# Optimization experiments

Hardware: AMD Instinct MI355X
Metric: run time of the kernel (lower is better)

## Reference

```python
import jax, jax.numpy as jnp
import numpy as np

K = 16
D_MODEL = 128

def _gather(pts, idx):
    # pts: [B,N,C], idx: [B,N,K] -> [B,N,K,C]
    return jax.vmap(lambda p, i: p[i])(pts, idx)

def setup_inputs() -> dict:
    key = jax.random.key(0)
    ks = jax.random.split(key, 20)
    s = 0.05
    def w(k_, shape):
        return jax.random.normal(k_, shape, dtype=jnp.float32) * s
    B, N, C = 4, 4096, 3
    TF, D = 128, D_MODEL
    return {
        "xyz": jax.random.normal(ks[0], (B, N, C), dtype=jnp.float32),
        "W0a": w(ks[1], (C, TF)),  "b0a": jnp.zeros((TF,), jnp.float32),
        "W0b": w(ks[2], (TF, TF)), "b0b": jnp.zeros((TF,), jnp.float32),
        "W1":  w(ks[3], (TF, D)),  "b1":  jnp.zeros((D,), jnp.float32),
        "W2":  w(ks[4], (D, TF)),  "b2":  jnp.zeros((TF,), jnp.float32),
        "Wd1": w(ks[5], (C, D)),   "bd1": jnp.zeros((D,), jnp.float32),
        "Wd2": w(ks[6], (D, D)),   "bd2": jnp.zeros((D,), jnp.float32),
        "Wg1": w(ks[7], (D, D)),   "bg1": jnp.zeros((D,), jnp.float32),
        "Wg2": w(ks[8], (D, D)),   "bg2": jnp.zeros((D,), jnp.float32),
        "Wq":  w(ks[9], (D, D)),
        "Wk":  w(ks[10], (D, D)),
        "Wv":  w(ks[11], (D, D)),
    }

def reference(xyz, W0a, b0a, W0b, b0b, W1, b1, W2, b2,
              Wd1, bd1, Wd2, bd2, Wg1, bg1, Wg2, bg2, Wq, Wk, Wv):
    sq = jnp.sum(xyz * xyz, axis=-1)
    dists = sq[:, :, None] - 2.0 * jnp.einsum('bnc,bmc->bnm', xyz, xyz) + sq[:, None, :]
    _, knn_idx = jax.lax.top_k(-dists, K)          # [B,N,K] nearest neighbors

    knn_xyz = _gather(xyz, knn_idx)                # [B,N,K,3]
    features = jax.nn.relu(xyz @ W0a + b0a) @ W0b + b0b   # fc0  [B,N,TF]
    pre = features
    x = features @ W1 + b1                          # fc1  [B,N,D]
    q = x @ Wq                                      # [B,N,D]
    kf = _gather(x @ Wk, knn_idx)                   # [B,N,K,D]
    vf = _gather(x @ Wv, knn_idx)                   # [B,N,K,D]

    delta = xyz[:, :, None, :] - knn_xyz            # [B,N,K,3]
    pos_enc = jax.nn.relu(delta @ Wd1 + bd1) @ Wd2 + bd2   # fc_delta [B,N,K,D]

    h = q[:, :, None, :] - kf + pos_enc
    attn_logits = jax.nn.relu(h @ Wg1 + bg1) @ Wg2 + bg2   # fc_gamma [B,N,K,D]
    attn = jax.nn.softmax(attn_logits / np.sqrt(D_MODEL).astype(np.float32), axis=-2)

    res = jnp.einsum('bmnf,bmnf->bmf', attn, vf + pos_enc)  # [B,N,D]
    res = res @ W2 + b2 + pre                               # [B,N,TF]
    return res, attn
```

## Files before the change

kernel.cpp:

```cpp
#include <hip/hip_runtime.h>
#include <math.h>

#define BB 4
#define NN 4096
#define KNNK 16
#define DD 128
#define BN (BB*NN)

typedef __attribute__((ext_vector_type(8))) short short8;
typedef __attribute__((ext_vector_type(4))) float floatx4;

__device__ __forceinline__ short f2bf(float x) {
  unsigned u = __float_as_uint(x);
  unsigned r = (u + 0x7fffu + ((u >> 16) & 1u)) >> 16;
  return (short)r;
}

__device__ __forceinline__ float bf2f(short h) {
  return __uint_as_float((unsigned)(unsigned short)h << 16);
}

__device__ __forceinline__ void mv16(const float* __restrict__ Wcol,
                                     const float* __restrict__ A,
                                     float acc[16]) {
#pragma unroll 2
  for (int f4 = 0; f4 < 32; ++f4) {
    float w0 = Wcol[(4 * f4 + 0) * 128];
    float w1 = Wcol[(4 * f4 + 1) * 128];
    float w2 = Wcol[(4 * f4 + 2) * 128];
    float w3 = Wcol[(4 * f4 + 3) * 128];
#pragma unroll
    for (int p = 0; p < 16; ++p) {
      float4 a = *reinterpret_cast<const float4*>(A + p * 128 + 4 * f4);
      acc[p] = fmaf(a.w, w3, fmaf(a.z, w2, fmaf(a.y, w1, fmaf(a.x, w0, acc[p]))));
    }
  }
}

__device__ __forceinline__ void ced(double& a, double& b) {
  double mn = fmin(a, b);
  double mx = fmax(a, b);
  a = mn;
  b = mx;
}

__device__ __forceinline__ void dsort16(double v[16]) {
#define CE(i, j) ced(v[i], v[j]);
  CE(0, 1) CE(2, 3) CE(4, 5) CE(6, 7) CE(8, 9) CE(10, 11) CE(12, 13) CE(14, 15)
  CE(0, 2) CE(1, 3) CE(4, 6) CE(5, 7) CE(8, 10) CE(9, 11) CE(12, 14) CE(13, 15)
  CE(1, 2) CE(5, 6) CE(9, 10) CE(13, 14)
  CE(0, 4) CE(1, 5) CE(2, 6) CE(3, 7) CE(8, 12) CE(9, 13) CE(10, 14) CE(11, 15)
  CE(2, 4) CE(3, 5) CE(10, 12) CE(11, 13)
  CE(1, 2) CE(3, 4) CE(5, 6) CE(9, 10) CE(11, 12) CE(13, 14)
  CE(0, 8) CE(1, 9) CE(2, 10) CE(3, 11) CE(4, 12) CE(5, 13) CE(6, 14) CE(7, 15)
  CE(4, 8) CE(5, 9) CE(6, 10) CE(7, 11)
  CE(2, 4) CE(3, 5) CE(6, 8) CE(7, 9) CE(10, 12) CE(11, 13)
  CE(1, 2) CE(3, 4) CE(5, 6) CE(7, 8) CE(9, 10) CE(11, 12) CE(13, 14)
#undef CE
}

__device__ __forceinline__ void dbitonic16(double m[16]) {
#pragma unroll
  for (int s = 8; s >= 1; s >>= 1) {
#pragma unroll
    for (int i = 0; i < 16; ++i) {
      if ((i & s) == 0) ced(m[i], m[i + s]);
    }
  }
}

__global__ __launch_bounds__(256, 4) void knn_kernel(const float* __restrict__ xyz,
                                                     int* __restrict__ knn) {
  const int wv = threadIdx.x >> 6;
  const int lane = threadIdx.x & 63;
  const int q = blockIdx.x * 4 + wv;
  const int b = q >> 12;
  const int n = q & 4095;
  const float* xb = xyz + (size_t)b * NN * 3;

  const float qx = xb[n * 3 + 0], qy = xb[n * 3 + 1], qz = xb[n * 3 + 2];
  const float qsq = __fadd_rn(__fadd_rn(__fmul_rn(qx, qx), __fmul_rn(qy, qy)),
                              __fmul_rn(qz, qz));

  double top[16];
#pragma unroll
  for (int batch = 0; batch < 4; ++batch) {
    double v[16];
#pragma unroll
    for (int i = 0; i < 16; ++i) {
      const int c = (batch * 16 + i) * 64 + lane;
      float cx = xb[c * 3 + 0], cy = xb[c * 3 + 1], cz = xb[c * 3 + 2];
      float csq = __fadd_rn(__fadd_rn(__fmul_rn(cx, cx), __fmul_rn(cy, cy)),
                            __fmul_rn(cz, cz));
      float dot = __fadd_rn(__fadd_rn(__fmul_rn(qx, cx), __fmul_rn(qy, cy)),
                            __fmul_rn(qz, cz));
      float d = __fadd_rn(__fsub_rn(qsq, __fmul_rn(2.0f, dot)), csq);
      unsigned u = __float_as_uint(d);
      u = (u & 0x80000000u) ? ~u : (u | 0x80000000u);
      unsigned long long key =
          0x3FF0000000000000ULL | (((unsigned long long)u << 12) | (unsigned)c);
      v[i] = __longlong_as_double((long long)key);
    }
    dsort16(v);
    if (batch == 0) {
#pragma unroll
      for (int i = 0; i < 16; ++i) top[i] = v[i];
    } else {
      double m[16];
#pragma unroll
      for (int i = 0; i < 16; ++i)
        m[i] = fmin(top[i], v[15 - i]);
      dbitonic16(m);
#pragma unroll
      for (int i = 0; i < 16; ++i) top[i] = m[i];
    }
  }

#pragma unroll
  for (int mask = 1; mask <= 32; mask <<= 1) {
    double oth[16];
#pragma unroll
    for (int i = 0; i < 16; ++i) {
      double y = __shfl_xor(top[15 - i], mask);
      oth[i] = fmin(y, top[i]);
    }
    dbitonic16(oth);
#pragma unroll
    for (int i = 0; i < 16; ++i) top[i] = oth[i];
  }

  if (lane == 0) {
    int* outp = knn + (size_t)q * KNNK;
#pragma unroll
    for (int k = 0; k < 16; ++k)
      outp[k] = (int)(__double_as_longlong(top[k]) & 0xFFFLL);
  }
}

__global__ void swz_kernel(const float* __restrict__ Wd2,
                           const float* __restrict__ Wg1,
                           const float* __restrict__ Wg2,
                           short* __restrict__ wsw) {
  int t = blockIdx.x * 256 + threadIdx.x;
  if (t >= 3 * 2048) return;
  int stage = t / 2048;
  int rem = t % 2048;
  int nt = rem / 256;
  int ks = (rem % 256) / 64;
  int lane = rem % 64;
  const float* W = (stage == 0) ? Wd2 : (stage == 1) ? Wg1 : Wg2;
  short8 o;
#pragma unroll
  for (int j = 0; j < 8; ++j) {
    int k = ks * 32 + (lane >> 4) * 8 + j;
    int n = nt * 16 + (lane & 15);
    o[j] = f2bf(W[k * 128 + n]);
  }
  *reinterpret_cast<short8*>(wsw + (size_t)t * 8) = o;
}

__global__ void swz2_kernel(const float* __restrict__ W0b,
                            const float* __restrict__ W1,
                            const float* __restrict__ Wq,
                            const float* __restrict__ Wk,
                            const float* __restrict__ Wv,
                            short* __restrict__ wsplit) {
  int t = blockIdx.x * 256 + threadIdx.x;
  if (t >= 5 * 2048) return;
  int mat = t / 2048;
  int rem = t % 2048;
  int lane = rem % 64;
  const float* W = (mat == 0) ? W0b : (mat == 1) ? W1 : (mat == 2) ? Wq
                   : (mat == 3) ? Wk : Wv;
  short8 hi, lo;
#pragma unroll
  for (int j = 0; j < 8; ++j) {
    int ks = (rem % 256) / 64;
    int nt = rem / 256;
    int k = ks * 32 + (lane >> 4) * 8 + j;
    int n = nt * 16 + (lane & 15);
    float w = W[k * 128 + n];
    short h = f2bf(w);
    hi[j] = h;
    lo[j] = f2bf(w - bf2f(h));
  }
  *reinterpret_cast<short8*>(wsplit + ((size_t)(2 * mat) * 2048 + rem) * 8) = hi;
  *reinterpret_cast<short8*>(wsplit + ((size_t)(2 * mat + 1) * 2048 + rem) * 8) = lo;
}

__global__ __launch_bounds__(256, 4) void point_mlp_mfma_kernel(
    const float* __restrict__ xyz, const float* __restrict__ W0a,
    const float* __restrict__ b0a, const float* __restrict__ b0b,
    const float* __restrict__ b1, const short* __restrict__ wsplit,
    float* __restrict__ pre, float* __restrict__ qv, float* __restrict__ kv,
    float* __restrict__ vv) {
  const int wv = threadIdx.x >> 6;
  const int lane = threadIdx.x & 63;
  const int g = lane >> 4;
  const int c = lane & 15;
  const int g0 = blockIdx.x * 16;
  const int nt0 = wv * 2;

  __shared__ __attribute__((aligned(16))) float trans[16 * 132];
  __shared__ float xs[64];
  if (threadIdx.x < 48) {
    int p = threadIdx.x / 3, cc = threadIdx.x % 3;
    xs[p * 4 + cc] = xyz[(size_t)(g0 + p) * 3 + cc];
  }
  __syncthreads();

  short8 ah[4], al[4];
  {
    const float x0 = xs[c * 4 + 0], x1 = xs[c * 4 + 1], x2 = xs[c * 4 + 2];
#pragma unroll
    for (int s = 0; s < 4; ++s) {
#pragma unroll
      for (int j = 0; j < 8; ++j) {
        const int k = s * 32 + g * 8 + j;
        float v = fmaf(x2, W0a[256 + k],
                       fmaf(x1, W0a[128 + k], fmaf(x0, W0a[k], b0a[k])));
        v = fmaxf(v, 0.f);
        const short h = f2bf(v);
        ah[s][j] = h;
        al[s][j] = f2bf(v - bf2f(h));
      }
    }
  }

#define DOGEMM(mat)                                                            \
  {                                                                            \
    const short* Bh = wsplit + (size_t)(2 * (mat)) * 16384;                    \
    const short* Bl = Bh + 16384;                                              \
    _Pragma("unroll") for (int ks = 0; ks < 4; ++ks) {                         \
      const size_t o0 = ((size_t)((nt0 + 0) * 4 + ks) * 64 + lane) * 8;        \
      const size_t o1 = ((size_t)((nt0 + 1) * 4 + ks) * 64 + lane) * 8;        \
      short8 bh0 = *reinterpret_cast<const short8*>(Bh + o0);                  \
      short8 bl0 = *reinterpret_cast<const short8*>(Bl + o0);                  \
      short8 bh1 = *reinterpret_cast<const short8*>(Bh + o1);                  \
      short8 bl1 = *reinterpret_cast<const short8*>(Bl + o1);                  \
      acc0 = __builtin_amdgcn_mfma_f32_16x16x32_bf16(ah[ks], bh0, acc0, 0, 0, 0); \
      acc1 = __builtin_amdgcn_mfma_f32_16x16x32_bf16(ah[ks], bh1, acc1, 0, 0, 0); \
      acc0 = __builtin_amdgcn_mfma_f32_16x16x32_bf16(ah[ks], bl0, acc0, 0, 0, 0); \
      acc1 = __builtin_amdgcn_mfma_f32_16x16x32_bf16(ah[ks], bl1, acc1, 0, 0, 0); \
      acc0 = __builtin_amdgcn_mfma_f32_16x16x32_bf16(al[ks], bh0, acc0, 0, 0, 0); \
      acc1 = __builtin_amdgcn_mfma_f32_16x16x32_bf16(al[ks], bh1, acc1, 0, 0, 0); \
    }                                                                          \
  }

#define SPLITLD()                                                              \
  _Pragma("unroll") for (int s = 0; s < 4; ++s) {                              \
    const float* p_ = &trans[c * 132 + s * 32 + g * 8];                        \
    float4 u0 = *reinterpret_cast<const float4*>(p_);                          \
    float4 u1 = *reinterpret_cast<const float4*>(p_ + 4);                      \
    float tmp[8] = {u0.x, u0.y, u0.z, u0.w, u1.x, u1.y, u1.z, u1.w};           \
    _Pragma("unroll") for (int j = 0; j < 8; ++j) {                            \
      short h_ = f2bf(tmp[j]);                                                 \
      ah[s][j] = h_;                                                           \
      al[s][j] = f2bf(tmp[j] - bf2f(h_));                                      \
    }                                                                          \
  }

  floatx4 acc0, acc1;
  const floatx4 zf = (floatx4){0.f, 0.f, 0.f, 0.f};

  acc0 = zf; acc1 = zf;
  DOGEMM(0);
  {
    const float bb0 = b0b[nt0 * 16 + c];
    const float bb1 = b0b[(nt0 + 1) * 16 + c];
#pragma unroll
    for (int r = 0; r < 4; ++r) {
      const int row = g * 4 + r;
      float v0 = acc0[r] + bb0;
      float v1 = acc1[r] + bb1;
      pre[(size_t)(g0 + row) * 128 + nt0 * 16 + c] = v0;
      pre[(size_t)(g0 + row) * 128 + (nt0 + 1) * 16 + c] = v1;
      trans[row * 132 + nt0 * 16 + c] = v0;
      trans[row * 132 + (nt0 + 1) * 16 + c] = v1;
    }
  }
  __syncthreads();
  SPLITLD();
  __syncthreads();

  acc0 = zf; acc1 = zf;
  DOGEMM(1);
  {
    const float bb0 = b1[nt0 * 16 + c];
    const float bb1 = b1[(nt0 + 1) * 16 + c];
#pragma unroll
    for (int r = 0; r < 4; ++r) {
      const int row = g * 4 + r;
      trans[row * 132 + nt0 * 16 + c] = acc0[r] + bb0;
      trans[row * 132 + (nt0 + 1) * 16 + c] = acc1[r] + bb1;
    }
  }
  __syncthreads();
  SPLITLD();
  __syncthreads();

#define GSTORE(dst)                                                            \
  _Pragma("unroll") for (int r = 0; r < 4; ++r) {                              \
    const int row = g0 + g * 4 + r;                                            \
    dst[(size_t)row * 128 + nt0 * 16 + c] = acc0[r];                           \
    dst[(size_t)row * 128 + (nt0 + 1) * 16 + c] = acc1[r];                     \
  }

  acc0 = zf; acc1 = zf;
  DOGEMM(2);
  GSTORE(qv);

  acc0 = zf; acc1 = zf;
  DOGEMM(3);
  GSTORE(kv);

  acc0 = zf; acc1 = zf;
  DOGEMM(4);
  GSTORE(vv);

#undef DOGEMM
#undef SPLITLD
#undef GSTORE
}

__global__ __launch_bounds__(256, 2) void attn_mfma_kernel(
    const float* __restrict__ xyz, const int* __restrict__ knn,
    const float* __restrict__ qv, const float* __restrict__ kv,
    const float* __restrict__ vv, const short* __restrict__ wsw,
    const float* __restrict__ Wd1, const float* __restrict__ bd1,
    const float* __restrict__ bd2, const float* __restrict__ bg1,
    const float* __restrict__ bg2, float* __restrict__ res_ws,
    float* __restrict__ out_attn) {
  const int wv = threadIdx.x >> 6;
  const int lane = threadIdx.x & 63;
  const int g = lane >> 4;
  const int c = lane & 15;
  const int bn = blockIdx.x * 4 + wv;
  const int b = bn >> 12;

  __shared__ __attribute__((aligned(16))) short conv[4][16 * 136];
  __shared__ int sidx[4][16];
  __shared__ float sdelta[4][64];

  if (lane < 16) sidx[wv][lane] = knn[(size_t)bn * 16 + lane];
  __syncthreads();
  if (lane < 48) {
    int k = lane / 3, cc = lane % 3;
    sdelta[wv][k * 4 + cc] = xyz[(size_t)bn * 3 + cc] -
                             xyz[((size_t)(b << 12) + sidx[wv][k]) * 3 + cc];
  }
  __syncthreads();

  short8 af[4];
  {
    float ddx = sdelta[wv][c * 4 + 0];
    float ddy = sdelta[wv][c * 4 + 1];
    float ddz = sdelta[wv][c * 4 + 2];
#pragma unroll
    for (int s = 0; s < 4; ++s) {
#pragma unroll
      for (int j = 0; j < 8; ++j) {
        int d = s * 32 + g * 8 + j;
        float v = fmaf(ddz, Wd1[256 + d],
                       fmaf(ddy, Wd1[128 + d], fmaf(ddx, Wd1[d], bd1[d])));
        af[s][j] = f2bf(fmaxf(v, 0.f));
      }
    }
  }

  float qc[8], bd2v[8], bg1v[8], bg2v[8];
#pragma unroll
  for (int nt = 0; nt < 8; ++nt) {
    qc[nt] = qv[(size_t)bn * 128 + nt * 16 + c];
    bd2v[nt] = bd2[nt * 16 + c];
    bg1v[nt] = bg1[nt * 16 + c];
    bg2v[nt] = bg2[nt * 16 + c];
  }

  floatx4 acc[8];

#pragma unroll
  for (int nt = 0; nt < 8; ++nt) acc[nt] = (floatx4){0.f, 0.f, 0.f, 0.f};
  {
    const short* Wst = wsw;
#pragma unroll
    for (int ks = 0; ks < 4; ++ks) {
#pragma unroll
      for (int nt = 0; nt < 8; ++nt) {
        short8 bf = *reinterpret_cast<const short8*>(
            Wst + ((size_t)(nt * 4 + ks) * 64 + lane) * 8);
        acc[nt] = __builtin_amdgcn_mfma_f32_16x16x32_bf16(af[ks], bf, acc[nt],
                                                          0, 0, 0);
      }
    }
  }

  float PE[8][4];
  int idxr[4];
#pragma unroll
  for (int r = 0; r < 4; ++r) idxr[r] = sidx[wv][g * 4 + r];
#pragma unroll
  for (int nt = 0; nt < 8; ++nt) {
#pragma unroll
    for (int r = 0; r < 4; ++r) {
      float pe = acc[nt][r] + bd2v[nt];
      PE[nt][r] = pe;
      float kvv = kv[((size_t)(b << 12) + idxr[r]) * 128 + nt * 16 + c];
      conv[wv][(g * 4 + r) * 136 + nt * 16 + c] = f2bf(qc[nt] - kvv + pe);
    }
  }
  __syncthreads();
#pragma unroll
  for (int s = 0; s < 4; ++s)
    af[s] = *reinterpret_cast<const short8*>(&conv[wv][c * 136 + s * 32 + g * 8]);
  __syncthreads();

#pragma unroll
  for (int nt = 0; nt < 8; ++nt) acc[nt] = (floatx4){0.f, 0.f, 0.f, 0.f};
  {
    const short* Wst = wsw + 16384;
#pragma unroll
    for (int ks = 0; ks < 4; ++ks) {
#pragma unroll
      for (int nt = 0; nt < 8; ++nt) {
        short8 bf = *reinterpret_cast<const short8*>(
            Wst + ((size_t)(nt * 4 + ks) * 64 + lane) * 8);
        acc[nt] = __builtin_amdgcn_mfma_f32_16x16x32_bf16(af[ks], bf, acc[nt],
                                                          0, 0, 0);
      }
    }
  }
#pragma unroll
  for (int nt = 0; nt < 8; ++nt) {
#pragma unroll
    for (int r = 0; r < 4; ++r) {
      conv[wv][(g * 4 + r) * 136 + nt * 16 + c] =
          f2bf(fmaxf(acc[nt][r] + bg1v[nt], 0.f));
    }
  }
  __syncthreads();
#pragma unroll
  for (int s = 0; s < 4; ++s)
    af[s] = *reinterpret_cast<const short8*>(&conv[wv][c * 136 + s * 32 + g * 8]);
  __syncthreads();

#pragma unroll
  for (int nt = 0; nt < 8; ++nt) acc[nt] = (floatx4){0.f, 0.f, 0.f, 0.f};
  {
    const short* Wst = wsw + 32768;
#pragma unroll
    for (int ks = 0; ks < 4; ++ks) {
#pragma unroll
      for (int nt = 0; nt < 8; ++nt) {
        short8 bf = *reinterpret_cast<const short8*>(
            Wst + ((size_t)(nt * 4 + ks) * 64 + lane) * 8);
        acc[nt] = __builtin_amdgcn_mfma_f32_16x16x32_bf16(af[ks], bf, acc[nt],
                                                          0, 0, 0);
      }
    }
  }

  const float inv = 0.0883883476483184f;
  float resv[8];
#pragma unroll
  for (int nt = 0; nt < 8; ++nt) {
    float l0 = (acc[nt][0] + bg2v[nt]) * inv;
    float l1 = (acc[nt][1] + bg2v[nt]) * inv;
    float l2 = (acc[nt][2] + bg2v[nt]) * inv;
    float l3 = (acc[nt][3] + bg2v[nt]) * inv;
    float m4 = fmaxf(fmaxf(l0, l1), fmaxf(l2, l3));
    m4 = fmaxf(m4, __shfl_xor(m4, 16));
    m4 = fmaxf(m4, __shfl_xor(m4, 32));
    float e0 = expf(l0 - m4), e1 = expf(l1 - m4);
    float e2 = expf(l2 - m4), e3 = expf(l3 - m4);
    float s4 = e0 + e1 + e2 + e3;
    s4 += __shfl_xor(s4, 16);
    s4 += __shfl_xor(s4, 32);
    float rs = 1.f / s4;
    float a0 = e0 * rs, a1 = e1 * rs, a2 = e2 * rs, a3 = e3 * rs;
    size_t base = ((size_t)bn * 16 + g * 4) * 128 + nt * 16 + c;
    out_attn[base + 0 * 128] = a0;
    out_attn[base + 1 * 128] = a1;
    out_attn[base + 2 * 128] = a2;
    out_attn[base + 3 * 128] = a3;
    float r = 0.f;
    {
      float v0 = vv[((size_t)(b << 12) + idxr[0]) * 128 + nt * 16 + c];
      float v1 = vv[((size_t)(b << 12) + idxr[1]) * 128 + nt * 16 + c];
      float v2 = vv[((size_t)(b << 12) + idxr[2]) * 128 + nt * 16 + c];
      float v3 = vv[((size_t)(b << 12) + idxr[3]) * 128 + nt * 16 + c];
      r = fmaf(a0, v0 + PE[nt][0], r);
      r = fmaf(a1, v1 + PE[nt][1], r);
      r = fmaf(a2, v2 + PE[nt][2], r);
      r = fmaf(a3, v3 + PE[nt][3], r);
    }
    r += __shfl_xor(r, 16);
    r += __shfl_xor(r, 32);
    resv[nt] = r;
  }
  if (g == 0) {
#pragma unroll
    for (int nt = 0; nt < 8; ++nt)
      res_ws[(size_t)bn * 128 + nt * 16 + c] = resv[nt];
  }
}

__global__ __launch_bounds__(128, 2) void epilogue_kernel(
    const float* __restrict__ res_ws, const float* __restrict__ W2,
    const float* __restrict__ b2, const float* __restrict__ pre,
    float* __restrict__ out_res) {
  const int t = threadIdx.x;
  const int g0 = blockIdx.x * 16;
  __shared__ __attribute__((aligned(16))) float buf[16 * 128];
#pragma unroll
  for (int p = 0; p < 16; ++p)
    buf[p * 128 + t] = res_ws[(size_t)(g0 + p) * 128 + t];
  __syncthreads();
  float acc[16];
  float bb = b2[t];
#pragma unroll
  for (int p = 0; p < 16; ++p)
    acc[p] = bb + pre[(size_t)(g0 + p) * 128 + t];
  mv16(W2 + t, buf, acc);
#pragma unroll
  for (int p = 0; p < 16; ++p)
    out_res[(size_t)(g0 + p) * 128 + t] = acc[p];
}

extern "C" void kernel_launch(void* const* d_in, const int* in_sizes, int n_in,
                              void* d_out, int out_size, void* d_ws,
                              size_t ws_size, hipStream_t stream) {
  const float* xyz = (const float*)d_in[0];
  const float* W0a = (const float*)d_in[1];
  const float* b0a = (const float*)d_in[2];
  const float* W0b = (const float*)d_in[3];
  const float* b0b = (const float*)d_in[4];
  const float* W1 = (const float*)d_in[5];
  const float* b1 = (const float*)d_in[6];
  const float* W2 = (const float*)d_in[7];
  const float* b2 = (const float*)d_in[8];
  const float* Wd1 = (const float*)d_in[9];
  const float* bd1 = (const float*)d_in[10];
  const float* Wd2 = (const float*)d_in[11];
  const float* bd2 = (const float*)d_in[12];
  const float* Wg1 = (const float*)d_in[13];
  const float* bg1 = (const float*)d_in[14];
  const float* Wg2 = (const float*)d_in[15];
  const float* bg2 = (const float*)d_in[16];
  const float* Wq = (const float*)d_in[17];
  const float* Wk = (const float*)d_in[18];
  const float* Wv = (const float*)d_in[19];

  char* ws = (char*)d_ws;
  int* knn = (int*)ws;
  float* pre = (float*)(ws + (1 << 20));
  float* qv = (float*)(ws + (9 << 20));
  float* kv = (float*)(ws + (17 << 20));
  float* vv = (float*)(ws + (25 << 20));
  float* res_ws = (float*)(ws + (33 << 20));
  short* wsw = (short*)(ws + (41 << 20));
  short* wsplit = (short*)(ws + (41 << 20) + (128 << 10));

  float* out_res = (float*)d_out;
  float* out_attn = out_res + (size_t)BN * DD;

  hipLaunchKernelGGL(swz_kernel, dim3(24), dim3(256), 0, stream, Wd2, Wg1, Wg2,
                     wsw);
  hipLaunchKernelGGL(swz2_kernel, dim3(40), dim3(256), 0, stream, W0b, W1, Wq,
                     Wk, Wv, wsplit);
  hipLaunchKernelGGL(knn_kernel, dim3(4096), dim3(256), 0, stream, xyz, knn);
  hipLaunchKernelGGL(point_mlp_mfma_kernel, dim3(1024), dim3(256), 0, stream,
                     xyz, W0a, b0a, b0b, b1, wsplit, pre, qv, kv, vv);
  hipLaunchKernelGGL(attn_mfma_kernel, dim3(4096), dim3(256), 0, stream, xyz,
                     knn, qv, kv, vv, wsw, Wd1, bd1, bd2, bg1, bg2, res_ws,
                     out_attn);
  hipLaunchKernelGGL(epilogue_kernel, dim3(1024), dim3(128), 0, stream, res_ws,
                     W2, b2, pre, out_res);
}
```

Measured before the change: 406.1 us.

## Move epilogue GEMM to split-bf16 MFMA, merge swizzle kernels, trim attn LDS syncs

The fp32 scalar W2 epilogue is replaced with an MFMA kernel that uses the same hi/lo bf16 split as the point MLP, with W2 now swizzled by a single merged weight-prep kernel. The attention kernel drops its shared-memory index and delta staging plus two barriers, prefetches the gathered k rows early, and raises launch bounds to 4 blocks per SM. Bias loads move later in the kernel to cut register pressure. The risks are higher register pressure from the kv prefetch under the tighter occupancy bound, and slight numeric differences from the split-bf16 epilogue.

Measured after the change: 381.0 us. -6.2%, faster.

```diff
diff --git a/kernel.cpp b/kernel.cpp
--- a/kernel.cpp
+++ b/kernel.cpp
@@ -20,20 +20,44 @@
   return __uint_as_float((unsigned)(unsigned short)h << 16);
 }
 
-__device__ __forceinline__ void mv16(const float* __restrict__ Wcol,
-                                     const float* __restrict__ A,
-                                     float acc[16]) {
-#pragma unroll 2
-  for (int f4 = 0; f4 < 32; ++f4) {
-    float w0 = Wcol[(4 * f4 + 0) * 128];
-    float w1 = Wcol[(4 * f4 + 1) * 128];
-    float w2 = Wcol[(4 * f4 + 2) * 128];
-    float w3 = Wcol[(4 * f4 + 3) * 128];
-#pragma unroll
-    for (int p = 0; p < 16; ++p) {
-      float4 a = *reinterpret_cast<const float4*>(A + p * 128 + 4 * f4);
-      acc[p] = fmaf(a.w, w3, fmaf(a.z, w2, fmaf(a.y, w1, fmaf(a.x, w0, acc[p]))));
-    }
+__device__ __forceinline__ void split_from_lds(const float* __restrict__ trans,
+                                               int c, int g, short8 ah[4],
+                                               short8 al[4]) {
+#pragma unroll
+  for (int s = 0; s < 4; ++s) {
+    const float* p_ = &trans[c * 132 + s * 32 + g * 8];
+    float4 u0 = *reinterpret_cast<const float4*>(p_);
+    float4 u1 = *reinterpret_cast<const float4*>(p_ + 4);
+    float tmp[8] = {u0.x, u0.y, u0.z, u0.w, u1.x, u1.y, u1.z, u1.w};
+#pragma unroll
+    for (int j = 0; j < 8; ++j) {
+      short h_ = f2bf(tmp[j]);
+      ah[s][j] = h_;
+      al[s][j] = f2bf(tmp[j] - bf2f(h_));
+    }
+  }
+}
+
+__device__ __forceinline__ void split_gemm2(const short* __restrict__ Bh,
+                                            int nt0, int lane,
+                                            const short8 ah[4],
+                                            const short8 al[4], floatx4& acc0,
+                                            floatx4& acc1) {
+  const short* Bl = Bh + 16384;
+#pragma unroll
+  for (int ks = 0; ks < 4; ++ks) {
+    const size_t o0 = ((size_t)((nt0 + 0) * 4 + ks) * 64 + lane) * 8;
+    const size_t o1 = ((size_t)((nt0 + 1) * 4 + ks) * 64 + lane) * 8;
+    short8 bh0 = *reinterpret_cast<const short8*>(Bh + o0);
+    short8 bl0 = *reinterpret_cast<const short8*>(Bl + o0);
+    short8 bh1 = *reinterpret_cast<const short8*>(Bh + o1);
+    short8 bl1 = *reinterpret_cast<const short8*>(Bl + o1);
+    acc0 = __builtin_amdgcn_mfma_f32_16x16x32_bf16(ah[ks], bh0, acc0, 0, 0, 0);
+    acc1 = __builtin_amdgcn_mfma_f32_16x16x32_bf16(ah[ks], bh1, acc1, 0, 0, 0);
+    acc0 = __builtin_amdgcn_mfma_f32_16x16x32_bf16(ah[ks], bl0, acc0, 0, 0, 0);
+    acc1 = __builtin_amdgcn_mfma_f32_16x16x32_bf16(ah[ks], bl1, acc1, 0, 0, 0);
+    acc0 = __builtin_amdgcn_mfma_f32_16x16x32_bf16(al[ks], bh0, acc0, 0, 0, 0);
+    acc1 = __builtin_amdgcn_mfma_f32_16x16x32_bf16(al[ks], bh1, acc1, 0, 0, 0);
   }
 }
 
@@ -137,55 +161,56 @@
   }
 }
 
-__global__ void swz_kernel(const float* __restrict__ Wd2,
-                           const float* __restrict__ Wg1,
-                           const float* __restrict__ Wg2,
-                           short* __restrict__ wsw) {
+__global__ void swz_all_kernel(const float* __restrict__ Wd2,
+                               const float* __restrict__ Wg1,
+                               const float* __restrict__ Wg2,
+                               const float* __restrict__ W0b,
+                               const float* __restrict__ W1,
+                               const float* __restrict__ Wq,
+                               const float* __restrict__ Wk,
+                               const float* __restrict__ Wv,
+                               const float* __restrict__ W2,
+                               short* __restrict__ wsw,
+                               short* __restrict__ wsplit) {
   int t = blockIdx.x * 256 + threadIdx.x;
-  if (t >= 3 * 2048) return;
-  int stage = t / 2048;
-  int rem = t % 2048;
-  int nt = rem / 256;
-  int ks = (rem % 256) / 64;
-  int lane = rem % 64;
-  const float* W = (stage == 0) ? Wd2 : (stage == 1) ? Wg1 : Wg2;
-  short8 o;
-#pragma unroll
-  for (int j = 0; j < 8; ++j) {
-    int k = ks * 32 + (lane >> 4) * 8 + j;
-    int n = nt * 16 + (lane & 15);
-    o[j] = f2bf(W[k * 128 + n]);
-  }
-  *reinterpret_cast<short8*>(wsw + (size_t)t * 8) = o;
-}
-
-__global__ void swz2_kernel(const float* __restrict__ W0b,
-                            const float* __restrict__ W1,
-                            const float* __restrict__ Wq,
-                            const float* __restrict__ Wk,
-                            const float* __restrict__ Wv,
-                            short* __restrict__ wsplit) {
-  int t = blockIdx.x * 256 + threadIdx.x;
-  if (t >= 5 * 2048) return;
-  int mat = t / 2048;
-  int rem = t % 2048;
-  int lane = rem % 64;
-  const float* W = (mat == 0) ? W0b : (mat == 1) ? W1 : (mat == 2) ? Wq
-                   : (mat == 3) ? Wk : Wv;
-  short8 hi, lo;
-#pragma unroll
-  for (int j = 0; j < 8; ++j) {
+  if (t < 3 * 2048) {
+    int stage = t / 2048;
+    int rem = t % 2048;
+    int nt = rem / 256;
     int ks = (rem % 256) / 64;
+    int lane = rem % 64;
+    const float* W = (stage == 0) ? Wd2 : (stage == 1) ? Wg1 : Wg2;
+    short8 o;
+#pragma unroll
+    for (int j = 0; j < 8; ++j) {
+      int k = ks * 32 + (lane >> 4) * 8 + j;
+      int n = nt * 16 + (lane & 15);
+      o[j] = f2bf(W[k * 128 + n]);
+    }
+    *reinterpret_cast<short8*>(wsw + (size_t)t * 8) = o;
+  } else {
+    int u = t - 3 * 2048;
+    if (u >= 6 * 2048) return;
+    int mat = u / 2048;
+    int rem = u % 2048;
     int nt = rem / 256;
-    int k = ks * 32 + (lane >> 4) * 8 + j;
-    int n = nt * 16 + (lane & 15);
-    float w = W[k * 128 + n];
-    short h = f2bf(w);
-    hi[j] = h;
-    lo[j] = f2bf(w - bf2f(h));
-  }
-  *reinterpret_cast<short8*>(wsplit + ((size_t)(2 * mat) * 2048 + rem) * 8) = hi;
-  *reinterpret_cast<short8*>(wsplit + ((size_t)(2 * mat + 1) * 2048 + rem) * 8) = lo;
+    int ks = (rem % 256) / 64;
+    int lane = rem % 64;
+    const float* W = (mat == 0) ? W0b : (mat == 1) ? W1 : (mat == 2) ? Wq
+                     : (mat == 3) ? Wk : (mat == 4) ? Wv : W2;
+    short8 hi, lo;
+#pragma unroll
+    for (int j = 0; j < 8; ++j) {
+      int k = ks * 32 + (lane >> 4) * 8 + j;
+      int n = nt * 16 + (lane & 15);
+      float w = W[k * 128 + n];
+      short h = f2bf(w);
+      hi[j] = h;
+      lo[j] = f2bf(w - bf2f(h));
+    }
+    *reinterpret_cast<short8*>(wsplit + ((size_t)(2 * mat) * 2048 + rem) * 8) = hi;
+    *reinterpret_cast<short8*>(wsplit + ((size_t)(2 * mat + 1) * 2048 + rem) * 8) = lo;
+  }
 }
 
 __global__ __launch_bounds__(256, 4) void point_mlp_mfma_kernel(
@@ -227,44 +252,11 @@
     }
   }
 
-#define DOGEMM(mat)                                                            \
-  {                                                                            \
-    const short* Bh = wsplit + (size_t)(2 * (mat)) * 16384;                    \
-    const short* Bl = Bh + 16384;                                              \
-    _Pragma("unroll") for (int ks = 0; ks < 4; ++ks) {                         \
-      const size_t o0 = ((size_t)((nt0 + 0) * 4 + ks) * 64 + lane) * 8;        \
-      const size_t o1 = ((size_t)((nt0 + 1) * 4 + ks) * 64 + lane) * 8;        \
-      short8 bh0 = *reinterpret_cast<const short8*>(Bh + o0);                  \
-      short8 bl0 = *reinterpret_cast<const short8*>(Bl + o0);                  \
-      short8 bh1 = *reinterpret_cast<const short8*>(Bh + o1);                  \
-      short8 bl1 = *reinterpret_cast<const short8*>(Bl + o1);                  \
-      acc0 = __builtin_amdgcn_mfma_f32_16x16x32_bf16(ah[ks], bh0, acc0, 0, 0, 0); \
-      acc1 = __builtin_amdgcn_mfma_f32_16x16x32_bf16(ah[ks], bh1, acc1, 0, 0, 0); \
-      acc0 = __builtin_amdgcn_mfma_f32_16x16x32_bf16(ah[ks], bl0, acc0, 0, 0, 0); \
-      acc1 = __builtin_amdgcn_mfma_f32_16x16x32_bf16(ah[ks], bl1, acc1, 0, 0, 0); \
-      acc0 = __builtin_amdgcn_mfma_f32_16x16x32_bf16(al[ks], bh0, acc0, 0, 0, 0); \
-      acc1 = __builtin_amdgcn_mfma_f32_16x16x32_bf16(al[ks], bh1, acc1, 0, 0, 0); \
-    }                                                                          \
-  }
-
-#define SPLITLD()                                                              \
-  _Pragma("unroll") for (int s = 0; s < 4; ++s) {                              \
-    const float* p_ = &trans[c * 132 + s * 32 + g * 8];                        \
-    float4 u0 = *reinterpret_cast<const float4*>(p_);                          \
-    float4 u1 = *reinterpret_cast<const float4*>(p_ + 4);                      \
-    float tmp[8] = {u0.x, u0.y, u0.z, u0.w, u1.x, u1.y, u1.z, u1.w};           \
-    _Pragma("unroll") for (int j = 0; j < 8; ++j) {                            \
-      short h_ = f2bf(tmp[j]);                                                 \
-      ah[s][j] = h_;                                                           \
-      al[s][j] = f2bf(tmp[j] - bf2f(h_));                                      \
-    }                                                                          \
-  }
-
   floatx4 acc0, acc1;
   const floatx4 zf = (floatx4){0.f, 0.f, 0.f, 0.f};
 
   acc0 = zf; acc1 = zf;
-  DOGEMM(0);
+  split_gemm2(wsplit + 0 * 32768, nt0, lane, ah, al, acc0, acc1);
   {
     const float bb0 = b0b[nt0 * 16 + c];
     const float bb1 = b0b[(nt0 + 1) * 16 + c];
@@ -280,11 +272,11 @@
     }
   }
   __syncthreads();
-  SPLITLD();
+  split_from_lds(trans, c, g, ah, al);
   __syncthreads();
 
   acc0 = zf; acc1 = zf;
-  DOGEMM(1);
+  split_gemm2(wsplit + 1 * 32768, nt0, lane, ah, al, acc0, acc1);
   {
     const float bb0 = b1[nt0 * 16 + c];
     const float bb1 = b1[(nt0 + 1) * 16 + c];
@@ -296,7 +288,7 @@
     }
   }
   __syncthreads();
-  SPLITLD();
+  split_from_lds(trans, c, g, ah, al);
   __syncthreads();
 
 #define GSTORE(dst)                                                            \
@@ -307,23 +299,21 @@
   }
 
   acc0 = zf; acc1 = zf;
-  DOGEMM(2);
+  split_gemm2(wsplit + 2 * 32768, nt0, lane, ah, al, acc0, acc1);
   GSTORE(qv);
 
   acc0 = zf; acc1 = zf;
-  DOGEMM(3);
+  split_gemm2(wsplit + 3 * 32768, nt0, lane, ah, al, acc0, acc1);
   GSTORE(kv);
 
   acc0 = zf; acc1 = zf;
-  DOGEMM(4);
+  split_gemm2(wsplit + 4 * 32768, nt0, lane, ah, al, acc0, acc1);
   GSTORE(vv);
 
-#undef DOGEMM
-#undef SPLITLD
 #undef GSTORE
 }
 
-__global__ __launch_bounds__(256, 2) void attn_mfma_kernel(
+__global__ __launch_bounds__(256, 4) void attn_mfma_kernel(
     const float* __restrict__ xyz, const int* __restrict__ knn,
     const float* __restrict__ qv, const float* __restrict__ kv,
     const float* __restrict__ vv, const short* __restrict__ wsw,
@@ -337,44 +327,44 @@
   const int c = lane & 15;
   const int bn = blockIdx.x * 4 + wv;
   const int b = bn >> 12;
+  const int base_n = b << 12;
 
   __shared__ __attribute__((aligned(16))) short conv[4][16 * 136];
-  __shared__ int sidx[4][16];
-  __shared__ float sdelta[4][64];
-
-  if (lane < 16) sidx[wv][lane] = knn[(size_t)bn * 16 + lane];
-  __syncthreads();
-  if (lane < 48) {
-    int k = lane / 3, cc = lane % 3;
-    sdelta[wv][k * 4 + cc] = xyz[(size_t)bn * 3 + cc] -
-                             xyz[((size_t)(b << 12) + sidx[wv][k]) * 3 + cc];
-  }
-  __syncthreads();
+
+  const int* knnp = knn + (size_t)bn * 16;
+  const int idxn = knnp[c];
+  int idxr[4];
+#pragma unroll
+  for (int r = 0; r < 4; ++r) idxr[r] = knnp[g * 4 + r];
+
+  float kvf[8][4];
+#pragma unroll
+  for (int nt = 0; nt < 8; ++nt)
+#pragma unroll
+    for (int r = 0; r < 4; ++r)
+      kvf[nt][r] = kv[((size_t)(base_n + idxr[r])) * 128 + nt * 16 + c];
+
+  const float ddx = xyz[(size_t)bn * 3 + 0] - xyz[((size_t)(base_n + idxn)) * 3 + 0];
+  const float ddy = xyz[(size_t)bn * 3 + 1] - xyz[((size_t)(base_n + idxn)) * 3 + 1];
+  const float ddz = xyz[(size_t)bn * 3 + 2] - xyz[((size_t)(base_n + idxn)) * 3 + 2];
 
   short8 af[4];
-  {
-    float ddx = sdelta[wv][c * 4 + 0];
-    float ddy = sdelta[wv][c * 4 + 1];
-    float ddz = sdelta[wv][c * 4 + 2];
-#pragma unroll
-    for (int s = 0; s < 4; ++s) {
-#pragma unroll
-      for (int j = 0; j < 8; ++j) {
-        int d = s * 32 + g * 8 + j;
-        float v = fmaf(ddz, Wd1[256 + d],
-                       fmaf(ddy, Wd1[128 + d], fmaf(ddx, Wd1[d], bd1[d])));
-        af[s][j] = f2bf(fmaxf(v, 0.f));
-      }
-    }
-  }
-
-  float qc[8], bd2v[8], bg1v[8], bg2v[8];
+#pragma unroll
+  for (int s = 0; s < 4; ++s) {
+#pragma unroll
+    for (int j = 0; j < 8; ++j) {
+      int d = s * 32 + g * 8 + j;
+      float v = fmaf(ddz, Wd1[256 + d],
+                     fmaf(ddy, Wd1[128 + d], fmaf(ddx, Wd1[d], bd1[d])));
+      af[s][j] = f2bf(fmaxf(v, 0.f));
+    }
+  }
+
+  float qc[8], bd2v[8];
 #pragma unroll
   for (int nt = 0; nt < 8; ++nt) {
     qc[nt] = qv[(size_t)bn * 128 + nt * 16 + c];
     bd2v[nt] = bd2[nt * 16 + c];
-    bg1v[nt] = bg1[nt * 16 + c];
-    bg2v[nt] = bg2[nt * 16 + c];
   }
 
   floatx4 acc[8];
@@ -396,17 +386,14 @@
   }
 
   float PE[8][4];
-  int idxr[4];
-#pragma unroll
-  for (int r = 0; r < 4; ++r) idxr[r] = sidx[wv][g * 4 + r];
 #pragma unroll
   for (int nt = 0; nt < 8; ++nt) {
 #pragma unroll
     for (int r = 0; r < 4; ++r) {
       float pe = acc[nt][r] + bd2v[nt];
       PE[nt][r] = pe;
-      float kvv = kv[((size_t)(b << 12) + idxr[r]) * 128 + nt * 16 + c];
-      conv[wv][(g * 4 + r) * 136 + nt * 16 + c] = f2bf(qc[nt] - kvv + pe);
+      conv[wv][(g * 4 + r) * 136 + nt * 16 + c] =
+          f2bf(qc[nt] - kvf[nt][r] + pe);
     }
   }
   __syncthreads();
@@ -432,10 +419,11 @@
   }
 #pragma unroll
   for (int nt = 0; nt < 8; ++nt) {
+    const float bg1v = bg1[nt * 16 + c];
 #pragma unroll
     for (int r = 0; r < 4; ++r) {
       conv[wv][(g * 4 + r) * 136 + nt * 16 + c] =
-          f2bf(fmaxf(acc[nt][r] + bg1v[nt], 0.f));
+          f2bf(fmaxf(acc[nt][r] + bg1v, 0.f));
     }
   }
   __syncthreads();
@@ -464,10 +452,11 @@
   float resv[8];
 #pragma unroll
   for (int nt = 0; nt < 8; ++nt) {
-    float l0 = (acc[nt][0] + bg2v[nt]) * inv;
-    float l1 = (acc[nt][1] + bg2v[nt]) * inv;
-    float l2 = (acc[nt][2] + bg2v[nt]) * inv;
-    float l3 = (acc[nt][3] + bg2v[nt]) * inv;
+    const float bg2v = bg2[nt * 16 + c];
+    float l0 = (acc[nt][0] + bg2v) * inv;
+    float l1 = (acc[nt][1] + bg2v) * inv;
+    float l2 = (acc[nt][2] + bg2v) * inv;
+    float l3 = (acc[nt][3] + bg2v) * inv;
     float m4 = fmaxf(fmaxf(l0, l1), fmaxf(l2, l3));
     m4 = fmaxf(m4, __shfl_xor(m4, 16));
     m4 = fmaxf(m4, __shfl_xor(m4, 32));
@@ -485,10 +474,10 @@
     out_attn[base + 3 * 128] = a3;
     float r = 0.f;
     {
-      float v0 = vv[((size_t)(b << 12) + idxr[0]) * 128 + nt * 16 + c];
-      float v1 = vv[((size_t)(b << 12) + idxr[1]) * 128 + nt * 16 + c];
-      float v2 = vv[((size_t)(b << 12) + idxr[2]) * 128 + nt * 16 + c];
-      float v3 = vv[((size_t)(b << 12) + idxr[3]) * 128 + nt * 16 + c];
+      float v0 = vv[((size_t)(base_n + idxr[0])) * 128 + nt * 16 + c];
+      float v1 = vv[((size_t)(base_n + idxr[1])) * 128 + nt * 16 + c];
+      float v2 = vv[((size_t)(base_n + idxr[2])) * 128 + nt * 16 + c];
+      float v3 = vv[((size_t)(base_n + idxr[3])) * 128 + nt * 16 + c];
       r = fmaf(a0, v0 + PE[nt][0], r);
       r = fmaf(a1, v1 + PE[nt][1], r);
       r = fmaf(a2, v2 + PE[nt][2], r);
@@ -505,26 +494,52 @@
   }
 }
 
-__global__ __launch_bounds__(128, 2) void epilogue_kernel(
-    const float* __restrict__ res_ws, const float* __restrict__ W2,
+__global__ __launch_bounds__(256, 4) void epilogue_mfma_kernel(
+    const float* __restrict__ res_ws, const short* __restrict__ wsplit,
     const float* __restrict__ b2, const float* __restrict__ pre,
     float* __restrict__ out_res) {
-  const int t = threadIdx.x;
+  const int wv = threadIdx.x >> 6;
+  const int lane = threadIdx.x & 63;
+  const int g = lane >> 4;
+  const int c = lane & 15;
   const int g0 = blockIdx.x * 16;
-  __shared__ __attribute__((aligned(16))) float buf[16 * 128];
-#pragma unroll
-  for (int p = 0; p < 16; ++p)
-    buf[p * 128 + t] = res_ws[(size_t)(g0 + p) * 128 + t];
-  __syncthreads();
-  float acc[16];
-  float bb = b2[t];
-#pragma unroll
-  for (int p = 0; p < 16; ++p)
-    acc[p] = bb + pre[(size_t)(g0 + p) * 128 + t];
-  mv16(W2 + t, buf, acc);
-#pragma unroll
-  for (int p = 0; p < 16; ++p)
-    out_res[(size_t)(g0 + p) * 128 + t] = acc[p];
+  const int nt0 = wv * 2;
+
+  __shared__ __attribute__((aligned(16))) float trans[16 * 132];
+
+#pragma unroll
+  for (int i = 0; i < 2; ++i) {
+    int idx4 = threadIdx.x + i * 256;
+    int row = idx4 >> 5;
+    int col4 = idx4 & 31;
+    float4 v = *reinterpret_cast<const float4*>(
+        res_ws + (size_t)(g0 + row) * 128 + col4 * 4);
+    *reinterpret_cast<float4*>(&trans[row * 132 + col4 * 4]) = v;
+  }
+  __syncthreads();
+
+  short8 ah[4], al[4];
+  split_from_lds(trans, c, g, ah, al);
+
+  float prv0[4], prv1[4];
+  const float bb0 = b2[nt0 * 16 + c];
+  const float bb1 = b2[(nt0 + 1) * 16 + c];
+#pragma unroll
+  for (int r = 0; r < 4; ++r) {
+    prv0[r] = pre[(size_t)(g0 + g * 4 + r) * 128 + nt0 * 16 + c];
+    prv1[r] = pre[(size_t)(g0 + g * 4 + r) * 128 + (nt0 + 1) * 16 + c];
+  }
+
+  floatx4 acc0 = (floatx4){0.f, 0.f, 0.f, 0.f};
+  floatx4 acc1 = (floatx4){0.f, 0.f, 0.f, 0.f};
+  split_gemm2(wsplit + 5 * 32768, nt0, lane, ah, al, acc0, acc1);
+
+#pragma unroll
+  for (int r = 0; r < 4; ++r) {
+    const int row = g0 + g * 4 + r;
+    out_res[(size_t)row * 128 + nt0 * 16 + c] = acc0[r] + bb0 + prv0[r];
+    out_res[(size_t)row * 128 + (nt0 + 1) * 16 + c] = acc1[r] + bb1 + prv1[r];
+  }
 }
 
 extern "C" void kernel_launch(void* const* d_in, const int* in_sizes, int n_in,
@@ -564,16 +579,14 @@
   float* out_res = (float*)d_out;
   float* out_attn = out_res + (size_t)BN * DD;
 
-  hipLaunchKernelGGL(swz_kernel, dim3(24), dim3(256), 0, stream, Wd2, Wg1, Wg2,
-                     wsw);
-  hipLaunchKernelGGL(swz2_kernel, dim3(40), dim3(256), 0, stream, W0b, W1, Wq,
-                     Wk, Wv, wsplit);
+  hipLaunchKernelGGL(swz_all_kernel, dim3(72), dim3(256), 0, stream, Wd2, Wg1,
+                     Wg2, W0b, W1, Wq, Wk, Wv, W2, wsw, wsplit);
   hipLaunchKernelGGL(knn_kernel, dim3(4096), dim3(256), 0, stream, xyz, knn);
   hipLaunchKernelGGL(point_mlp_mfma_kernel, dim3(1024), dim3(256), 0, stream,
                      xyz, W0a, b0a, b0b, b1, wsplit, pre, qv, kv, vv);
   hipLaunchKernelGGL(attn_mfma_kernel, dim3(4096), dim3(256), 0, stream, xyz,
                      knn, qv, kv, vv, wsw, Wd1, bd1, bd2, bg1, bg2, res_ws,
                      out_attn);
-  hipLaunchKernelGGL(epilogue_kernel, dim3(1024), dim3(128), 0, stream, res_ws,
-                     W2, b2, pre, out_res);
-}
+  hipLaunchKernelGGL(epilogue_mfma_kernel, dim3(1024), dim3(256), 0, stream,
+                     res_ws, wsplit, b2, pre, out_res);
+}
```
